# Kernel tuning notes

Measured on AMD Instinct MI355X. Metric: run time of the kernel, lower is better.

Reference implementation:

```python
import jax, jax.numpy as jnp
import numpy as np

B = 128
IN_FEATURES = 1024
HIDDEN = 512
N_OPS = 2        # operators = [T_Norm.min, T_Conorm.max]
N_EDGE_TYPES = 2 # [no_edge, normal_edge]
NO_EDGE_OFFSET_T_NORM = 1.0
NO_EDGE_OFFSET_T_CONORM = 0.0


def setup_inputs() -> dict:
    key = jax.random.key(0)
    x = jax.random.uniform(key, (B, IN_FEATURES), dtype=jnp.float32)
    sizes = [IN_FEATURES, HIDDEN, IN_FEATURES]
    inp = {"x": x}
    for li in range(len(sizes) - 1):
        fi, fo = sizes[li], sizes[li + 1]
        # counts are initialized to ones in the torch module (buffers, not trained by grad)
        inp[f"etc{li}"] = jnp.ones((fo, N_OPS, fi, N_EDGE_TYPES), dtype=jnp.float32)
        inp[f"otc{li}"] = jnp.ones((fo, N_OPS), dtype=jnp.float32)
    return inp


def _layer_forward(key, x, edge_type_count, operator_type_count):
    # x: [B, in]; edge_type_count: [out, n_ops, in, n_et]; operator_type_count: [out, n_ops]
    k_op, k_edge = jax.random.split(key)
    # hard gumbel-softmax == argmax over (logits + gumbel noise), tau irrelevant for argmax
    g_op = jax.random.gumbel(k_op, operator_type_count.shape, dtype=jnp.float32)
    op_idx = jnp.argmax(operator_type_count + g_op, axis=-1)          # [out], 0=min(T_Norm), 1=max(T_Conorm)
    g_e = jax.random.gumbel(k_edge, edge_type_count.shape, dtype=jnp.float32)
    sel_idx = jnp.argmax(edge_type_count + g_e, axis=-1)              # [out, n_ops, in]
    sel = jax.nn.one_hot(sel_idx, N_EDGE_TYPES, dtype=x.dtype)        # [out, n_ops, in, n_et]
    # edge_selection = op_edge_selection[range(out), op_indices]
    out_f = sel.shape[0]
    edge_sel = sel[jnp.arange(out_f), op_idx]                         # [out, in, n_et]
    # edge_type_values: no_edge -> 0 (+1 offset if operator is T_Norm/min), normal_edge -> x
    no_edge_val = jnp.where(op_idx == 0, NO_EDGE_OFFSET_T_NORM, NO_EDGE_OFFSET_T_CONORM)  # [out]
    a = edge_sel[..., 0] * no_edge_val[:, None]                       # [out, in]
    b = edge_sel[None, :, :, 1] * x[:, None, :]                       # [B, out, in]
    edge_values = jnp.maximum(a[None, :, :], b)                       # max over edge-type dim (one-hot -> 2 terms)
    out_min = jnp.min(edge_values, axis=-1)                           # [B, out]
    out_max = jnp.max(edge_values, axis=-1)                           # [B, out]
    return jnp.where(op_idx[None, :] == 0, out_min, out_max)


def reference(x, etc0, otc0, etc1, otc1):
    base = jax.random.key(42)
    h = _layer_forward(jax.random.fold_in(base, 0), x, etc0, otc0)
    out = _layer_forward(jax.random.fold_in(base, 1), h, etc1, otc1)
    return out
```

## Files before the change

kernel.cpp:

```cpp
#include <hip/hip_runtime.h>
#include <stdint.h>


__host__ __device__ inline uint32_t rotl32(uint32_t x, uint32_t d) {
  return (x << d) | (x >> (32u - d));
}

__host__ __device__ inline void threefry2x32(uint32_t k0, uint32_t k1,
                                             uint32_t x0, uint32_t x1,
                                             uint32_t* o0, uint32_t* o1) {
  uint32_t ks0 = k0, ks1 = k1, ks2 = k0 ^ k1 ^ 0x1BD11BDAu;
  x0 += ks0; x1 += ks1;
#define TF_R(r) { x0 += x1; x1 = rotl32(x1, r); x1 ^= x0; }
  TF_R(13u) TF_R(15u) TF_R(26u) TF_R(6u)
  x0 += ks1; x1 += ks2 + 1u;
  TF_R(17u) TF_R(29u) TF_R(16u) TF_R(24u)
  x0 += ks2; x1 += ks0 + 2u;
  TF_R(13u) TF_R(15u) TF_R(26u) TF_R(6u)
  x0 += ks0; x1 += ks1 + 3u;
  TF_R(17u) TF_R(29u) TF_R(16u) TF_R(24u)
  x0 += ks1; x1 += ks2 + 4u;
  TF_R(13u) TF_R(15u) TF_R(26u) TF_R(6u)
  x0 += ks2; x1 += ks0 + 5u;
#undef TF_R
  *o0 = x0; *o1 = x1;
}

__device__ __forceinline__ uint32_t rbits32(uint32_t k0, uint32_t k1,
                                            uint32_t e) {
  uint32_t a, b;
  threefry2x32(k0, k1, 0u, e, &a, &b);
  return a ^ b;
}

__device__ __forceinline__ double flog(double x) {
  long long bits = __double_as_longlong(x);
  int e = (int)(bits >> 52) - 1023;
  double m = __longlong_as_double((bits & 0x000fffffffffffffLL) |
                                  0x3ff0000000000000LL);
  if (m > 1.4142135623730951) { m *= 0.5; e += 1; }
  double mp1 = m + 1.0;
  double r = __builtin_amdgcn_rcp(mp1);
  r = r * __builtin_fma(-mp1, r, 2.0);
  r = r * __builtin_fma(-mp1, r, 2.0);
  double z = (m - 1.0) * r;
  double w = z * z;
  double p = 1.0 / 15.0;
  p = __builtin_fma(p, w, 1.0 / 13.0);
  p = __builtin_fma(p, w, 1.0 / 11.0);
  p = __builtin_fma(p, w, 1.0 / 9.0);
  p = __builtin_fma(p, w, 1.0 / 7.0);
  p = __builtin_fma(p, w, 1.0 / 5.0);
  p = __builtin_fma(p, w, 1.0 / 3.0);
  p = __builtin_fma(p, w, 1.0);
  double de = (double)e;
  const double ln2_hi = 6.93147180369123816490e-01;
  const double ln2_lo = 1.90821492927058770002e-10;
  return __builtin_fma(de, ln2_hi,
                       __builtin_fma(2.0 * z, p, de * ln2_lo));
}

__device__ __forceinline__ float gumbel_from_u32(uint32_t bits) {
  uint32_t fb = (bits >> 9) | 0x3f800000u;
  float f = __uint_as_float(fb) - 1.0f;
  float u = (f > 0.0f) ? f : 1.17549435e-38f;
  float l1 = (float)flog((double)u);
  float l2 = (float)flog((double)(-l1));
  return -l2;
}

__device__ __forceinline__ float fast_ln(float x) {
  uint32_t b = __float_as_uint(x);
  int e = (int)(b >> 23) - 127;
  float m = __uint_as_float((b & 0x007fffffu) | 0x3f800000u);
  if (m > 1.41421356f) { m *= 0.5f; e += 1; }
  float z = (m - 1.0f) * __builtin_amdgcn_rcpf(m + 1.0f);
  float w = z * z;
  float p = __builtin_fmaf(w, __builtin_fmaf(w, 0.14285715f, 0.2f),
                           0.33333334f);
  float q = __builtin_fmaf(w, p, 1.0f);
  float lnm = 2.0f * z * q;
  return __builtin_fmaf((float)e, 0.69314718f, lnm);
}

__device__ __forceinline__ float gumbel_fast(uint32_t bits) {
  uint32_t fb = (bits >> 9) | 0x3f800000u;
  float f = __uint_as_float(fb) - 1.0f;
  float u = (f > 0.0f) ? f : 1.17549435e-38f;
  float l1 = fast_ln(u);
  return -fast_ln(-l1);
}

__device__ __forceinline__ float guard_tau(float a, float b) {
  return 1e-3f + 3.1e-5f * (fabsf(a) + fabsf(b));
}

__device__ __noinline__ bool sel_exact(float c0, float c1,
                                       uint32_t r0, uint32_t r1) {
  return (c1 + gumbel_from_u32(r1)) > (c0 + gumbel_from_u32(r0));
}

__device__ __forceinline__ bool sel_guarded(float c0, float c1,
                                            uint32_t r0, uint32_t r1) {
  float t0 = c0 + gumbel_fast(r0);
  float t1 = c1 + gumbel_fast(r1);
  float diff = t1 - t0;
  if (__builtin_expect(fabsf(diff) <= guard_tau(t0, t1), 0))
    return sel_exact(c0, c1, r0, r1);
  return diff > 0.0f;
}

__device__ __forceinline__ bool sel_cmp(float c0, float c1,
                                        uint32_t r0, uint32_t r1) {
  if (__builtin_expect(c0 == c1, 1)) {
    int gap = (int)(r1 >> 9) - (int)(r0 >> 9);
    int T = 8 + (int)((fabsf(c0) + 16.0f) * 3.0f);
    if (__builtin_expect(gap >= T || gap <= -T, 1)) return gap > 0;
    return sel_guarded(c0, c1, r0, r1);
  }
  return sel_guarded(c0, c1, r0, r1);
}

__global__ __launch_bounds__(256) void edges_kernel(
    const float* __restrict__ etcA, const float* __restrict__ otcA,
    uint32_t oa0, uint32_t oa1, uint32_t ea0, uint32_t ea1,
    int* __restrict__ opA, unsigned long long* __restrict__ selA,
    const float* __restrict__ etcB, const float* __restrict__ otcB,
    uint32_t ob0, uint32_t ob1, uint32_t eb0, uint32_t eb1,
    int* __restrict__ opB, unsigned long long* __restrict__ selB) {
  int widx = threadIdx.x >> 6;
  int lane = threadIdx.x & 63;
  const float *etc, *otc; unsigned long long* selw; int* opx;
  uint32_t ok0, ok1, k0, k1;
  int inlog, o, ibase, wordbase;
  bool store_op;
  if (blockIdx.x < 512) {
    etc = etcA; otc = otcA; opx = opA; selw = selA;
    ok0 = oa0; ok1 = oa1; k0 = ea0; k1 = ea1; inlog = 10;
    o = blockIdx.x;
    ibase = widx * 256;
    wordbase = o * 16 + widx * 4;
    store_op = (threadIdx.x == 0);
  } else {
    etc = etcB; otc = otcB; opx = opB; selw = selB;
    ok0 = ob0; ok1 = ob1; k0 = eb0; k1 = eb1; inlog = 9;
    int bb = blockIdx.x - 512;
    o = bb * 2 + (widx >> 1);
    ibase = (widx & 1) * 256;
    wordbase = o * 8 + (widx & 1) * 4;
    store_op = ((widx & 1) == 0) && (lane == 0);
  }

  uint32_t rop = 0; float cop = 0.0f;
  if (lane < 2) {
    rop = rbits32(ok0, ok1, (uint32_t)(2 * o + lane));
    cop = otc[2 * o + lane];
  }
  uint32_t rop0 = (uint32_t)__shfl((int)rop, 0, 64);
  uint32_t rop1 = (uint32_t)__shfl((int)rop, 1, 64);
  float cop0 = __shfl(cop, 0, 64);
  float cop1 = __shfl(cop, 1, 64);
  int j = sel_cmp(cop0, cop1, rop0, rop1) ? 1 : 0;
  if (store_op) opx[o] = j;

  uint32_t ebase = (uint32_t)((o * 2 + j) << (inlog + 1));
  const float* cbase = etc + (size_t)ebase;
  bool selv[4];
#pragma unroll
  for (int p = 0; p < 4; ++p) {
    int i = ibase + p * 64 + lane;
    uint32_t e0 = ebase + (uint32_t)(2 * i);
    uint32_t r0 = rbits32(k0, k1, e0);
    uint32_t r1 = rbits32(k0, k1, e0 + 1u);
    float2 cc = *(const float2*)(cbase + 2 * i);
    selv[p] = sel_cmp(cc.x, cc.y, r0, r1);
  }
#pragma unroll
  for (int p = 0; p < 4; ++p) {
    unsigned long long m = __ballot(selv[p] ? 1 : 0);
    if (lane == 0) selw[wordbase + p] = m;
  }
}

template <int IN_F, int OUT_F>
__global__ __launch_bounds__(256) void forward_kernel(
    const float* __restrict__ x, const int* __restrict__ opidx,
    const unsigned long long* __restrict__ selw, float* __restrict__ out) {
  constexpr int W32 = IN_F / 32;
  constexpr int CH = IN_F / 256;
  const uint32_t* __restrict__ sel32 = (const uint32_t*)selw;
  int wave = blockIdx.x * 4 + (threadIdx.x >> 6);
  int lane = threadIdx.x & 63;
  int og = wave % (OUT_F / 8);
  int b  = wave / (OUT_F / 8);
  int o0 = og * 8;
  int sh = (lane * 4) & 31;
  int wb = lane >> 3;

  float sgn[8], neu[8];
  int opv[8];
#pragma unroll
  for (int jj = 0; jj < 8; ++jj) {
    int op = opidx[o0 + jj];
    opv[jj] = op;
    sgn[jj] = op ? 1.0f : -1.0f;
    neu[jj] = op ? 0.0f : -1.0f;
  }
  float acc[8];
#pragma unroll
  for (int jj = 0; jj < 8; ++jj) acc[jj] = -1e30f;
  const float* xrow = x + (size_t)b * IN_F;
#pragma unroll
  for (int cc = 0; cc < CH; ++cc) {
    int i0 = cc * 256 + lane * 4;
    float4 xv = *(const float4*)(xrow + i0);
    int w32 = cc * 8 + wb;
#pragma unroll
    for (int jj = 0; jj < 8; ++jj) {
      uint32_t m32 = sel32[(o0 + jj) * W32 + w32];
      uint32_t b4 = (m32 >> sh) & 0xFu;
      float s = sgn[jj], n = neu[jj];
      float v0 = (b4 & 1u) ? s * xv.x : n;
      float v1 = (b4 & 2u) ? s * xv.y : n;
      float v2 = (b4 & 4u) ? s * xv.z : n;
      float v3 = (b4 & 8u) ? s * xv.w : n;
      acc[jj] = fmaxf(acc[jj], fmaxf(fmaxf(v0, v1), fmaxf(v2, v3)));
    }
  }
#pragma unroll
  for (int d = 1; d < 64; d <<= 1) {
#pragma unroll
    for (int jj = 0; jj < 8; ++jj)
      acc[jj] = fmaxf(acc[jj], __shfl_xor(acc[jj], d, 64));
  }
  if (lane == 0) {
    float4 r0, r1;
    r0.x = opv[0] ? acc[0] : -acc[0];
    r0.y = opv[1] ? acc[1] : -acc[1];
    r0.z = opv[2] ? acc[2] : -acc[2];
    r0.w = opv[3] ? acc[3] : -acc[3];
    r1.x = opv[4] ? acc[4] : -acc[4];
    r1.y = opv[5] ? acc[5] : -acc[5];
    r1.z = opv[6] ? acc[6] : -acc[6];
    r1.w = opv[7] ? acc[7] : -acc[7];
    float* op = out + (size_t)b * OUT_F + o0;
    *(float4*)op = r0;
    *(float4*)(op + 4) = r1;
  }
}

extern "C" void kernel_launch(void* const* d_in, const int* in_sizes, int n_in,
                              void* d_out, int out_size, void* d_ws, size_t ws_size,
                              hipStream_t stream) {
  const float* x    = (const float*)d_in[0];
  const float* etc0 = (const float*)d_in[1];
  const float* otc0 = (const float*)d_in[2];
  const float* etc1 = (const float*)d_in[3];
  const float* otc1 = (const float*)d_in[4];
  float* out = (float*)d_out;

  uint32_t K0a, K0b, K1a, K1b;
  threefry2x32(0u, 42u, 0u, 0u, &K0a, &K0b);
  threefry2x32(0u, 42u, 0u, 1u, &K1a, &K1b);
  uint32_t op0k0, op0k1, ed0k0, ed0k1;
  threefry2x32(K0a, K0b, 0u, 0u, &op0k0, &op0k1);
  threefry2x32(K0a, K0b, 0u, 1u, &ed0k0, &ed0k1);
  uint32_t op1k0, op1k1, ed1k0, ed1k1;
  threefry2x32(K1a, K1b, 0u, 0u, &op1k0, &op1k1);
  threefry2x32(K1a, K1b, 0u, 1u, &ed1k0, &ed1k1);

  char* wsb = (char*)d_ws;
  int* opidx0 = (int*)wsb;
  int* opidx1 = (int*)(wsb + 2048);
  unsigned long long* selw0 = (unsigned long long*)(wsb + 8192);
  unsigned long long* selw1 = (unsigned long long*)(wsb + 8192 + 65536);
  float* h = (float*)(wsb + 8192 + 131072);

  hipLaunchKernelGGL(edges_kernel, dim3(1024), dim3(256), 0, stream,
                     etc0, otc0, op0k0, op0k1, ed0k0, ed0k1, opidx0, selw0,
                     etc1, otc1, op1k0, op1k1, ed1k0, ed1k1, opidx1, selw1);
  hipLaunchKernelGGL((forward_kernel<1024, 512>), dim3(2048), dim3(256), 0,
                     stream, x, opidx0, selw0, h);
  hipLaunchKernelGGL((forward_kernel<512, 1024>), dim3(4096), dim3(256), 0,
                     stream, h, opidx1, selw1, out);
}
```

Measured before the change: 100.1 us.

## Store edge masks as wave-uniform 64-bit SGPR masks and select with v_cndmask

The edges kernel now writes selection bits in a layout where each 32-bit ballot half is duplicated into a 64-bit word. The forward kernel can then load each mask as a scalar and feed it straight to v_cndmask as the lane condition. The forward kernel also processes two batch rows per wave, one per half-wave, and branches on the per-output operator to do a direct min or max with the right neutral value. This removes the sign-flip arithmetic and the per-lane bit extraction. The cost is twice the mask storage, half as many blocks, and inline asm that relies on the masks being wave-uniform.

Measured after the change: 100.6 us. About the same (+0.5%).

```diff
diff --git a/kernel.cpp b/kernel.cpp
--- a/kernel.cpp
+++ b/kernel.cpp
@@ -121,33 +121,39 @@
   return sel_guarded(c0, c1, r0, r1);
 }
 
+__device__ __forceinline__ unsigned long long dup32(uint32_t v) {
+  return ((unsigned long long)v << 32) | (unsigned long long)v;
+}
+
 __global__ __launch_bounds__(256) void edges_kernel(
     const float* __restrict__ etcA, const float* __restrict__ otcA,
     uint32_t oa0, uint32_t oa1, uint32_t ea0, uint32_t ea1,
-    int* __restrict__ opA, unsigned long long* __restrict__ selA,
+    int* __restrict__ opA, unsigned long long* __restrict__ mtA,
     const float* __restrict__ etcB, const float* __restrict__ otcB,
     uint32_t ob0, uint32_t ob1, uint32_t eb0, uint32_t eb1,
-    int* __restrict__ opB, unsigned long long* __restrict__ selB) {
+    int* __restrict__ opB, unsigned long long* __restrict__ mtB) {
   int widx = threadIdx.x >> 6;
   int lane = threadIdx.x & 63;
-  const float *etc, *otc; unsigned long long* selw; int* opx;
+  int il = lane & 31;
+  int half = lane >> 5;
+  const float *etc, *otc; unsigned long long* mt; int* opx;
   uint32_t ok0, ok1, k0, k1;
-  int inlog, o, ibase, wordbase;
+  int inlog, o, ibase, c0;
   bool store_op;
   if (blockIdx.x < 512) {
-    etc = etcA; otc = otcA; opx = opA; selw = selA;
+    etc = etcA; otc = otcA; opx = opA; mt = mtA;
     ok0 = oa0; ok1 = oa1; k0 = ea0; k1 = ea1; inlog = 10;
     o = blockIdx.x;
     ibase = widx * 256;
-    wordbase = o * 16 + widx * 4;
+    c0 = (o * 8 + widx * 2);
     store_op = (threadIdx.x == 0);
   } else {
-    etc = etcB; otc = otcB; opx = opB; selw = selB;
+    etc = etcB; otc = otcB; opx = opB; mt = mtB;
     ok0 = ob0; ok1 = ob1; k0 = eb0; k1 = eb1; inlog = 9;
     int bb = blockIdx.x - 512;
     o = bb * 2 + (widx >> 1);
     ibase = (widx & 1) * 256;
-    wordbase = o * 8 + (widx & 1) * 4;
+    c0 = (o * 4 + (widx & 1) * 2);
     store_op = ((widx & 1) == 0) && (lane == 0);
   }
 
@@ -164,88 +170,98 @@
   if (store_op) opx[o] = j;
 
   uint32_t ebase = (uint32_t)((o * 2 + j) << (inlog + 1));
-  const float* cbase = etc + (size_t)ebase;
-  bool selv[4];
-#pragma unroll
-  for (int p = 0; p < 4; ++p) {
-    int i = ibase + p * 64 + lane;
-    uint32_t e0 = ebase + (uint32_t)(2 * i);
-    uint32_t r0 = rbits32(k0, k1, e0);
-    uint32_t r1 = rbits32(k0, k1, e0 + 1u);
-    float2 cc = *(const float2*)(cbase + 2 * i);
-    selv[p] = sel_cmp(cc.x, cc.y, r0, r1);
-  }
-#pragma unroll
-  for (int p = 0; p < 4; ++p) {
-    unsigned long long m = __ballot(selv[p] ? 1 : 0);
-    if (lane == 0) selw[wordbase + p] = m;
+  int ioff = ibase + half * 128 + il * 4;
+  const float* cb = etc + (size_t)ebase + 2 * ioff;
+  float4 ca = *(const float4*)cb;
+  float4 cbv = *(const float4*)(cb + 4);
+  uint32_t e0 = ebase + (uint32_t)(2 * ioff);
+  bool s0 = sel_cmp(ca.x, ca.y, rbits32(k0, k1, e0 + 0u), rbits32(k0, k1, e0 + 1u));
+  bool s1 = sel_cmp(ca.z, ca.w, rbits32(k0, k1, e0 + 2u), rbits32(k0, k1, e0 + 3u));
+  bool s2 = sel_cmp(cbv.x, cbv.y, rbits32(k0, k1, e0 + 4u), rbits32(k0, k1, e0 + 5u));
+  bool s3 = sel_cmp(cbv.z, cbv.w, rbits32(k0, k1, e0 + 6u), rbits32(k0, k1, e0 + 7u));
+  unsigned long long b0 = __ballot(s0 ? 1 : 0);
+  unsigned long long b1 = __ballot(s1 ? 1 : 0);
+  unsigned long long b2 = __ballot(s2 ? 1 : 0);
+  unsigned long long b3 = __ballot(s3 ? 1 : 0);
+  if (lane == 0) {
+    unsigned long long* w = mt + (size_t)c0 * 4;
+    w[0] = dup32((uint32_t)b0);  w[4 + 0] = dup32((uint32_t)(b0 >> 32));
+    w[1] = dup32((uint32_t)b1);  w[4 + 1] = dup32((uint32_t)(b1 >> 32));
+    w[2] = dup32((uint32_t)b2);  w[4 + 2] = dup32((uint32_t)(b2 >> 32));
+    w[3] = dup32((uint32_t)b3);  w[4 + 3] = dup32((uint32_t)(b3 >> 32));
   }
 }
 
 template <int IN_F, int OUT_F>
 __global__ __launch_bounds__(256) void forward_kernel(
     const float* __restrict__ x, const int* __restrict__ opidx,
-    const unsigned long long* __restrict__ selw, float* __restrict__ out) {
-  constexpr int W32 = IN_F / 32;
-  constexpr int CH = IN_F / 256;
-  const uint32_t* __restrict__ sel32 = (const uint32_t*)selw;
-  int wave = blockIdx.x * 4 + (threadIdx.x >> 6);
+    const unsigned long long* __restrict__ maskT, float* __restrict__ out) {
+  constexpr int CH = IN_F / 128;
+  int wu = __builtin_amdgcn_readfirstlane(threadIdx.x >> 6);
+  int gwave = blockIdx.x * 4 + wu;
+  int og = gwave & (OUT_F / 8 - 1);
+  int bg = gwave >> (OUT_F == 512 ? 6 : 7);
+  int o0 = og * 8;
   int lane = threadIdx.x & 63;
-  int og = wave % (OUT_F / 8);
-  int b  = wave / (OUT_F / 8);
-  int o0 = og * 8;
-  int sh = (lane * 4) & 31;
-  int wb = lane >> 3;
-
-  float sgn[8], neu[8];
-  int opv[8];
-#pragma unroll
-  for (int jj = 0; jj < 8; ++jj) {
-    int op = opidx[o0 + jj];
-    opv[jj] = op;
-    sgn[jj] = op ? 1.0f : -1.0f;
-    neu[jj] = op ? 0.0f : -1.0f;
-  }
-  float acc[8];
-#pragma unroll
-  for (int jj = 0; jj < 8; ++jj) acc[jj] = -1e30f;
+  int il = lane & 31;
+  int b = bg * 2 + (lane >> 5);
+
   const float* xrow = x + (size_t)b * IN_F;
-#pragma unroll
-  for (int cc = 0; cc < CH; ++cc) {
-    int i0 = cc * 256 + lane * 4;
-    float4 xv = *(const float4*)(xrow + i0);
-    int w32 = cc * 8 + wb;
-#pragma unroll
-    for (int jj = 0; jj < 8; ++jj) {
-      uint32_t m32 = sel32[(o0 + jj) * W32 + w32];
-      uint32_t b4 = (m32 >> sh) & 0xFu;
-      float s = sgn[jj], n = neu[jj];
-      float v0 = (b4 & 1u) ? s * xv.x : n;
-      float v1 = (b4 & 2u) ? s * xv.y : n;
-      float v2 = (b4 & 4u) ? s * xv.z : n;
-      float v3 = (b4 & 8u) ? s * xv.w : n;
-      acc[jj] = fmaxf(acc[jj], fmaxf(fmaxf(v0, v1), fmaxf(v2, v3)));
+  float4 xv[CH];
+#pragma unroll
+  for (int c = 0; c < CH; ++c)
+    xv[c] = *(const float4*)(xrow + c * 128 + il * 4);
+
+  float res[8];
+#pragma unroll
+  for (int j = 0; j < 8; ++j) {
+    int op = opidx[o0 + j];
+    const unsigned long long* mp = maskT + (size_t)(o0 + j) * (CH * 4);
+    float acc;
+    if (op) {
+      acc = 0.0f;
+#pragma unroll
+      for (int c = 0; c < CH; ++c) {
+        unsigned long long m0 = mp[c * 4 + 0], m1 = mp[c * 4 + 1];
+        unsigned long long m2 = mp[c * 4 + 2], m3 = mp[c * 4 + 3];
+        float v0, v1, v2, v3;
+        asm("v_cndmask_b32 %0, 0, %1, %2" : "=v"(v0) : "v"(xv[c].x), "s"(m0));
+        asm("v_cndmask_b32 %0, 0, %1, %2" : "=v"(v1) : "v"(xv[c].y), "s"(m1));
+        asm("v_cndmask_b32 %0, 0, %1, %2" : "=v"(v2) : "v"(xv[c].z), "s"(m2));
+        asm("v_cndmask_b32 %0, 0, %1, %2" : "=v"(v3) : "v"(xv[c].w), "s"(m3));
+        acc = fmaxf(acc, fmaxf(v0, v1));
+        acc = fmaxf(acc, fmaxf(v2, v3));
+      }
+#pragma unroll
+      for (int d = 1; d < 32; d <<= 1)
+        acc = fmaxf(acc, __shfl_xor(acc, d, 64));
+    } else {
+      acc = 1.0f;
+#pragma unroll
+      for (int c = 0; c < CH; ++c) {
+        unsigned long long m0 = mp[c * 4 + 0], m1 = mp[c * 4 + 1];
+        unsigned long long m2 = mp[c * 4 + 2], m3 = mp[c * 4 + 3];
+        float v0, v1, v2, v3;
+        asm("v_cndmask_b32 %0, 1.0, %1, %2" : "=v"(v0) : "v"(xv[c].x), "s"(m0));
+        asm("v_cndmask_b32 %0, 1.0, %1, %2" : "=v"(v1) : "v"(xv[c].y), "s"(m1));
+        asm("v_cndmask_b32 %0, 1.0, %1, %2" : "=v"(v2) : "v"(xv[c].z), "s"(m2));
+        asm("v_cndmask_b32 %0, 1.0, %1, %2" : "=v"(v3) : "v"(xv[c].w), "s"(m3));
+        acc = fminf(acc, fminf(v0, v1));
+        acc = fminf(acc, fminf(v2, v3));
+      }
+#pragma unroll
+      for (int d = 1; d < 32; d <<= 1)
+        acc = fminf(acc, __shfl_xor(acc, d, 64));
     }
-  }
-#pragma unroll
-  for (int d = 1; d < 64; d <<= 1) {
-#pragma unroll
-    for (int jj = 0; jj < 8; ++jj)
-      acc[jj] = fmaxf(acc[jj], __shfl_xor(acc[jj], d, 64));
-  }
-  if (lane == 0) {
+    res[j] = acc;
+  }
+  if (il == 0) {
     float4 r0, r1;
-    r0.x = opv[0] ? acc[0] : -acc[0];
-    r0.y = opv[1] ? acc[1] : -acc[1];
-    r0.z = opv[2] ? acc[2] : -acc[2];
-    r0.w = opv[3] ? acc[3] : -acc[3];
-    r1.x = opv[4] ? acc[4] : -acc[4];
-    r1.y = opv[5] ? acc[5] : -acc[5];
-    r1.z = opv[6] ? acc[6] : -acc[6];
-    r1.w = opv[7] ? acc[7] : -acc[7];
-    float* op = out + (size_t)b * OUT_F + o0;
-    *(float4*)op = r0;
-    *(float4*)(op + 4) = r1;
+    r0.x = res[0]; r0.y = res[1]; r0.z = res[2]; r0.w = res[3];
+    r1.x = res[4]; r1.y = res[5]; r1.z = res[6]; r1.w = res[7];
+    float* po = out + (size_t)b * OUT_F + o0;
+    *(float4*)po = r0;
+    *(float4*)(po + 4) = r1;
   }
 }
 
@@ -272,15 +288,15 @@
   char* wsb = (char*)d_ws;
   int* opidx0 = (int*)wsb;
   int* opidx1 = (int*)(wsb + 2048);
-  unsigned long long* selw0 = (unsigned long long*)(wsb + 8192);
-  unsigned long long* selw1 = (unsigned long long*)(wsb + 8192 + 65536);
-  float* h = (float*)(wsb + 8192 + 131072);
+  unsigned long long* mt0 = (unsigned long long*)(wsb + 8192);
+  unsigned long long* mt1 = (unsigned long long*)(wsb + 8192 + 131072);
+  float* h = (float*)(wsb + 8192 + 262144);
 
   hipLaunchKernelGGL(edges_kernel, dim3(1024), dim3(256), 0, stream,
-                     etc0, otc0, op0k0, op0k1, ed0k0, ed0k1, opidx0, selw0,
-                     etc1, otc1, op1k0, op1k1, ed1k0, ed1k1, opidx1, selw1);
-  hipLaunchKernelGGL((forward_kernel<1024, 512>), dim3(2048), dim3(256), 0,
-                     stream, x, opidx0, selw0, h);
-  hipLaunchKernelGGL((forward_kernel<512, 1024>), dim3(4096), dim3(256), 0,
-                     stream, h, opidx1, selw1, out);
-}
+                     etc0, otc0, op0k0, op0k1, ed0k0, ed0k1, opidx0, mt0,
+                     etc1, otc1, op1k0, op1k1, ed1k0, ed1k1, opidx1, mt1);
+  hipLaunchKernelGGL((forward_kernel<1024, 512>), dim3(1024), dim3(256), 0,
+                     stream, x, opidx0, mt0, h);
+  hipLaunchKernelGGL((forward_kernel<512, 1024>), dim3(2048), dim3(256), 0,
+                     stream, h, opidx1, mt1, out);
+}
```
